# Performance work log

Measured on AMD Instinct MI355X. Metric: run time of the kernel, lower is better.

Reference implementation:

```python
import jax, jax.numpy as jnp
import numpy as np


def setup_inputs() -> dict:
    key = jax.random.key(0)
    k1, k2, k3, k4 = jax.random.split(key, 4)
    B, T, K = 256, 2048, 48
    logits = jax.random.normal(k1, (B, T, K), dtype=jnp.float32)
    transition_params = jax.random.normal(k2, (K, K), dtype=jnp.float32)
    targets = jax.random.randint(k3, (B, T), 0, K, dtype=jnp.int32)
    input_lengths = jax.random.randint(k4, (B,), 0, T, dtype=jnp.int32)
    return {"logits": logits, "transition_params": transition_params,
            "targets": targets, "input_lengths": input_lengths}


def _crf_log_likelihood(logits, transition_params, targets, input_lengths):
    B, T, K = logits.shape
    mask = (jnp.arange(T)[None, :] < input_lengths[:, None]).astype(logits.dtype)  # [B,T]

    # unary score: gather logits at target tags, masked sum over time
    unary = jnp.take_along_axis(logits, targets[..., None].astype(jnp.int32), axis=2)[..., 0]  # [B,T]
    unary_score = jnp.sum(unary * mask, axis=1)

    # binary score: transitions between consecutive tags, masked by mask[:,1:]
    binary = transition_params[targets[:, :-1], targets[:, 1:]]  # [B,T-1]
    binary_score = jnp.sum(binary * mask[:, 1:], axis=1)

    # log norm via forward algorithm (sequential logsumexp scan)
    alpha0 = logits[:, 0, :]  # [B,K]

    def step(alpha, logit_t):
        # alpha: [B,K] prev tag scores; logit_t: [B,K]
        scores = alpha[:, :, None] + transition_params[None, :, :]  # [B,K,K]
        new_alpha = logit_t + jax.nn.logsumexp(scores, axis=1)      # [B,K]
        return new_alpha, new_alpha

    _, alphas_rest = jax.lax.scan(step, alpha0, jnp.swapaxes(logits[:, 1:, :], 0, 1))
    all_alphas = jnp.concatenate([alpha0[None], alphas_rest], axis=0)  # [T,B,K]
    all_alphas = jnp.swapaxes(all_alphas, 0, 1)                        # [B,T,K]

    last_index = jnp.maximum(0, input_lengths - 1).astype(jnp.int32)   # [B]
    final_alpha = jnp.take_along_axis(all_alphas, last_index[:, None, None], axis=1)[:, 0, :]  # [B,K]
    log_norm = jax.nn.logsumexp(final_alpha, axis=1)
    log_norm = jnp.where(input_lengths <= 0, jnp.zeros_like(log_norm), log_norm)

    return unary_score + binary_score - log_norm  # [B]


def reference(logits, transition_params, targets, input_lengths):
    return _crf_log_likelihood(logits, transition_params, targets, input_lengths)
```

## Files before the change

kernel.cpp:

```cpp
#include <hip/hip_runtime.h>
#include <hip/hip_bf16.h>
#include <math.h>

#define TT   2048
#define KK   48
#define KP   68

typedef __attribute__((ext_vector_type(8))) short bf16x8;
typedef __attribute__((ext_vector_type(4))) float f32x4;
typedef __attribute__((ext_vector_type(2))) float f32x2;
typedef __attribute__((ext_vector_type(4))) unsigned int u32x4;
typedef unsigned short ushort_t;

union FragU { u32x4 u; bf16x8 h; };
union Q4   { f32x4 v; f32x2 h[2]; };

__device__ __forceinline__ float rlf(float x, int l) {
    return __uint_as_float((unsigned)__builtin_amdgcn_readlane((int)__float_as_uint(x), l));
}
__device__ __forceinline__ unsigned pk2(float a, float b) {
    __hip_bfloat162 h = __float22bfloat162_rn(make_float2(a, b));
    return *(unsigned*)&h;
}
__device__ __forceinline__ unsigned pk2a(float a, float b) {
    unsigned r;
    asm("v_cvt_pk_bf16_f32 %0, %1, %2" : "=v"(r) : "v"(a), "v"(b));
    return r;
}
__device__ __forceinline__ f32x2 pkmul(f32x2 a, f32x2 b) {
    f32x2 d;
    asm("v_pk_mul_f32 %0, %1, %2" : "=v"(d) : "v"(a), "v"(b));
    return d;
}

template <int SEGT, int NSEGT>
__global__ __launch_bounds__(64, 4) void crf_seg_kernel(
    const float* __restrict__ logits,
    const float* __restrict__ trans,
    const int*   __restrict__ lens,
    ushort_t*    __restrict__ Qout,
    float*       __restrict__ sigout)
{
    constexpr int NFULLT = NSEGT - 1;
    const int b    = blockIdx.x;
    const int seg  = blockIdx.y;
    const int job  = b * NSEGT + seg;
    const int lane = threadIdx.x;
    const int c = lane & 15, g = lane >> 4;

    int t0, t1;
    if (seg < NFULLT) { t0 = SEGT * seg + 1; t1 = SEGT * seg + SEGT; }
    else {
        int L  = lens[b];
        int nf = (L >= 2) ? (L - 1) / SEGT : 0;
        if (nf > NFULLT) nf = NFULLT;
        t0 = SEGT * nf + 1; t1 = L - 1;
    }

    __shared__ float    eLs[2][64];
    __shared__ ushort_t Qst[KK * KP];

    FragU A[3][2];
    #pragma unroll
    for (int mt = 0; mt < 3; ++mt) {
        const int r = 16 * mt + c;
        #pragma unroll
        for (int q = 0; q < 2; ++q) {
            #pragma unroll
            for (int ep = 0; ep < 4; ++ep) {
                float v0, v1;
                { int e = 2 * ep;     int kk = 32 * q + 16 * (e >> 2) + 4 * g + (e & 3);
                  v0 = (kk < KK) ? __expf(trans[kk * KK + r]) : 0.f; }
                { int e = 2 * ep + 1; int kk = 32 * q + 16 * (e >> 2) + 4 * g + (e & 3);
                  v1 = (kk < KK) ? __expf(trans[kk * KK + r]) : 0.f; }
                A[mt][q].u[ep] = pk2(v0, v1);
            }
        }
    }

    FragU Bf[3][2];
    #pragma unroll
    for (int nt = 0; nt < 3; ++nt) {
        const int n = 16 * nt + c;
        #pragma unroll
        for (int q = 0; q < 2; ++q) {
            #pragma unroll
            for (int ep = 0; ep < 4; ++ep) {
                int e0 = 2 * ep, e1 = 2 * ep + 1;
                int k0 = 32 * q + 16 * (e0 >> 2) + 4 * g + (e0 & 3);
                int k1 = 32 * q + 16 * (e1 >> 2) + 4 * g + (e1 & 3);
                unsigned lo = (k0 == n) ? 0x3F80u : 0u;
                unsigned hi = (k1 == n) ? 0x3F80u : 0u;
                Bf[nt][q].u[ep] = (hi << 16) | lo;
            }
        }
    }

    const float* lg_b = logits + (size_t)b * TT * KK;
    const int jj = (lane < KK) ? lane : 0;
    float sg = 0.f;
    const int nsteps = t1 - t0 + 1;

    f32x4 z4 = {0.f, 0.f, 0.f, 0.f};
    asm("" : "+v"(z4));

#define COLX(nt_, FIRST_)                                                     \
    {                                                                         \
        f32x4 y0 = __builtin_amdgcn_mfma_f32_16x16x32_bf16(                   \
                       A[0][0].h, Bf[nt_][0].h, z4, 0, 0, 0);                 \
        y0 = __builtin_amdgcn_mfma_f32_16x16x32_bf16(                         \
                       A[0][1].h, Bf[nt_][1].h, y0, 0, 0, 0);                 \
        f32x4 y1 = __builtin_amdgcn_mfma_f32_16x16x32_bf16(                   \
                       A[1][0].h, Bf[nt_][0].h, z4, 0, 0, 0);                 \
        y1 = __builtin_amdgcn_mfma_f32_16x16x32_bf16(                         \
                       A[1][1].h, Bf[nt_][1].h, y1, 0, 0, 0);                 \
        f32x4 y2 = __builtin_amdgcn_mfma_f32_16x16x32_bf16(                   \
                       A[2][0].h, Bf[nt_][0].h, z4, 0, 0, 0);                 \
        y2 = __builtin_amdgcn_mfma_f32_16x16x32_bf16(                         \
                       A[2][1].h, Bf[nt_][1].h, y2, 0, 0, 0);                 \
        if (FIRST_) {                                                         \
            float r = __uint_as_float((unsigned)                              \
                __builtin_amdgcn_readfirstlane((int)__float_as_uint(y0[0]))); \
            float rr = __builtin_amdgcn_rcpf(r);                              \
            sg += jk ? 0.f : __logf(r);                                       \
            rr2[0] = rr; rr2[1] = rr;                                         \
            { Q4 t_; t_.v = eL4[0]; es0.h[0] = pkmul(t_.h[0], rr2);           \
                                    es0.h[1] = pkmul(t_.h[1], rr2); }         \
            { Q4 t_; t_.v = eL4[1]; es1.h[0] = pkmul(t_.h[0], rr2);           \
                                    es1.h[1] = pkmul(t_.h[1], rr2); }         \
            { Q4 t_; t_.v = eL4[2]; es2.h[0] = pkmul(t_.h[0], rr2);           \
                                    es2.h[1] = pkmul(t_.h[1], rr2); }         \
        }                                                                     \
        Q4 q0_, q1_, q2_;                                                     \
        q0_.v = y0; q1_.v = y1; q2_.v = y2;                                   \
        f32x2 v00 = pkmul(q0_.h[0], es0.h[0]);                                \
        f32x2 v01 = pkmul(q0_.h[1], es0.h[1]);                                \
        f32x2 v10 = pkmul(q1_.h[0], es1.h[0]);                                \
        f32x2 v11 = pkmul(q1_.h[1], es1.h[1]);                                \
        f32x2 v20 = pkmul(q2_.h[0], es2.h[0]);                                \
        f32x2 v21 = pkmul(q2_.h[1], es2.h[1]);                                \
        unsigned w0 = pk2a(v00[0], v00[1]);                                   \
        unsigned w1 = pk2a(v01[0], v01[1]);                                   \
        unsigned w2 = pk2a(v10[0], v10[1]);                                   \
        unsigned w3 = pk2a(v11[0], v11[1]);                                   \
        unsigned w4 = pk2a(v20[0], v20[1]);                                   \
        unsigned w5 = pk2a(v21[0], v21[1]);                                   \
        if (G_) {                                                             \
            Bf[nt_][0].u[0] = jk ? Bf[nt_][0].u[0] : w0;                      \
            Bf[nt_][0].u[1] = jk ? Bf[nt_][0].u[1] : w1;                      \
            Bf[nt_][0].u[2] = jk ? Bf[nt_][0].u[2] : w2;                      \
            Bf[nt_][0].u[3] = jk ? Bf[nt_][0].u[3] : w3;                      \
            Bf[nt_][1].u[0] = jk ? Bf[nt_][1].u[0] : w4;                      \
            Bf[nt_][1].u[1] = jk ? Bf[nt_][1].u[1] : w5;                      \
        } else {                                                              \
            Bf[nt_][0].u[0] = w0; Bf[nt_][0].u[1] = w1;                       \
            Bf[nt_][0].u[2] = w2; Bf[nt_][0].u[3] = w3;                       \
            Bf[nt_][1].u[0] = w4; Bf[nt_][1].u[1] = w5;                       \
        }                                                                     \
        Bf[nt_][1].u[2] = 0u; Bf[nt_][1].u[3] = 0u;                           \
    }

#define STEP(u_, GG_)                                                         \
    {                                                                         \
        constexpr bool G_ = (GG_);                                            \
        const int i = 8 * cs + (u_);                                          \
        f32x4 eL4[3];                                                         \
        _Pragma("unroll")                                                     \
        for (int mt = 0; mt < 3; ++mt)                                        \
            eL4[mt] = *(const f32x4*)&eLs[par][16 * mt + 4 * g];              \
        float lgn = pf[((u_) + 1) & 7];                                       \
        int nr = t0 + i + 9; if (nr > TT - 1) nr = TT - 1;                    \
        pf[((u_) + 1) & 7] = lg_b[nr * KK + jj];                              \
        if (lane < KK) eLs[par ^ 1][lane] = __expf(lgn);                      \
        const bool jk = G_ ? (i >= nsteps) : false;                           \
        f32x2 rr2;                                                            \
        Q4 es0, es1, es2;                                                     \
        COLX(0, 1)                                                            \
        COLX(1, 0)                                                            \
        COLX(2, 0)                                                            \
        par ^= 1;                                                             \
    }

    int par = 0;
    if (nsteps > 0) {
        if (lane < KK) eLs[0][lane] = __expf(lg_b[t0 * KK + jj]);
        float pf[8];
        #pragma unroll
        for (int j = 1; j < 8; ++j) {
            int rj = t0 + j; if (rj > TT - 1) rj = TT - 1;
            pf[j] = lg_b[rj * KK + jj];
        }
        { int rj = t0 + 8; if (rj > TT - 1) rj = TT - 1; pf[0] = lg_b[rj * KK + jj]; }

        const int nchunks = (nsteps + 7) / 8;
        #pragma unroll 1
        for (int cs = 0; cs < nchunks - 1; ++cs) {
            STEP(0, false) STEP(1, false) STEP(2, false) STEP(3, false)
            STEP(4, false) STEP(5, false) STEP(6, false) STEP(7, false)
        }
        {
            const int cs = nchunks - 1;
            STEP(0, true) STEP(1, true) STEP(2, true) STEP(3, true)
            STEP(4, true) STEP(5, true) STEP(6, true) STEP(7, true)
        }
    }
#undef STEP
#undef COLX

    #pragma unroll
    for (int nt = 0; nt < 3; ++nt) {
        ushort_t* basep = &Qst[(16 * nt + c) * KP];
        *(unsigned*)&basep[4 * g]          = Bf[nt][0].u[0];
        *(unsigned*)&basep[4 * g + 2]      = Bf[nt][0].u[1];
        *(unsigned*)&basep[16 + 4 * g]     = Bf[nt][0].u[2];
        *(unsigned*)&basep[16 + 4 * g + 2] = Bf[nt][0].u[3];
        *(unsigned*)&basep[32 + 4 * g]     = Bf[nt][1].u[0];
        *(unsigned*)&basep[32 + 4 * g + 2] = Bf[nt][1].u[1];
    }
    __syncthreads();

    if (lane < KK) {
        const int m = lane;
        unsigned w[24];
        #pragma unroll
        for (int np = 0; np < 24; ++np) {
            unsigned lo = Qst[(2 * np)     * KP + m];
            unsigned hi = Qst[(2 * np + 1) * KP + m];
            w[np] = (hi << 16) | lo;
        }
        ushort_t* dst = Qout + (size_t)job * (KK * KK) + m * KK;
        #pragma unroll
        for (int i4 = 0; i4 < 6; ++i4) {
            uint4 o; o.x = w[4*i4]; o.y = w[4*i4+1]; o.z = w[4*i4+2]; o.w = w[4*i4+3];
            *(uint4*)&dst[8 * i4] = o;
        }
    }
    if (lane == 0) sigout[job] = sg;
}

template <int SEGT, int NSEGT>
__global__ __launch_bounds__(64) void crf_comb_kernel(
    const float* __restrict__ logits, const float* __restrict__ trans,
    const int* __restrict__ targets, const int* __restrict__ lens,
    const ushort_t* __restrict__ Qall, const float* __restrict__ sig,
    float* __restrict__ out)
{
    constexpr int NFULLT = NSEGT - 1;
    const int b = blockIdx.x, lane = threadIdx.x;
    const int jj = (lane < KK) ? lane : 0;
    const int L = lens[b];

    __shared__ float s_trans[KK * KK];
    for (int k = lane; k < KK * KK; k += 64) s_trans[k] = trans[k];
    __syncthreads();

    const float* lg_b = logits  + (size_t)b * TT * KK;
    const int*   tg_b = targets + (size_t)b * TT;

    float ub = 0.f;
    #pragma unroll 4
    for (int t = lane; t < TT; t += 64) {
        if (t < L) {
            int tg = tg_b[t];
            ub += lg_b[t * KK + tg];
            if (t >= 1) { int tp = tg_b[t - 1]; ub += s_trans[tp * KK + tg]; }
        }
    }
    #pragma unroll
    for (int d = 32; d >= 1; d >>= 1) ub += __shfl_xor(ub, d, 64);

    float log_norm = 0.f;
    if (L > 0) {
        float a0 = lg_b[jj];
        float M  = rlf(a0, 0);
        float s  = (lane < KK) ? __expf(a0 - M) : 0.f;
        int nf = (L >= 2) ? (L - 1) / SEGT : 0;
        if (nf > NFULLT) nf = NFULLT;

        for (int ci = 0; ci <= nf; ++ci) {
            const int job = b * NSEGT + ((ci < nf) ? ci : NFULLT);
            const ushort_t* Qr = Qall + (size_t)job * (KK * KK) + jj * KK;
            unsigned rw[24];
            #pragma unroll
            for (int i4 = 0; i4 < 6; ++i4) {
                uint4 v = *(const uint4*)&Qr[8 * i4];
                rw[4*i4] = v.x; rw[4*i4+1] = v.y; rw[4*i4+2] = v.z; rw[4*i4+3] = v.w;
            }
            float acc = 0.f;
            #pragma unroll
            for (int ip = 0; ip < 24; ++ip) {
                unsigned u = rw[ip];
                float q0 = __uint_as_float(u << 16);
                float q1 = __uint_as_float(u & 0xFFFF0000u);
                acc = fmaf(rlf(s, 2 * ip),     q0, acc);
                acc = fmaf(rlf(s, 2 * ip + 1), q1, acc);
            }
            float r  = rlf(acc, 0);
            float rr = __builtin_amdgcn_rcpf(r);
            s = (lane < KK) ? acc * rr : 0.f;
            M += __logf(r) + sig[job];
        }

        float ssum = (lane < KK) ? s : 0.f;
        #pragma unroll
        for (int d = 32; d >= 1; d >>= 1) ssum += __shfl_xor(ssum, d, 64);
        log_norm = M + __logf(ssum);
    }

    if (lane == 0) out[b] = (L <= 0) ? 0.f : (ub - log_norm);
}

__global__ __launch_bounds__(64) void crf_fwd_fallback(
    const float* __restrict__ logits, const float* __restrict__ trans,
    const int* __restrict__ targets, const int* __restrict__ lens,
    float* __restrict__ out)
{
    const int b = blockIdx.x, lane = threadIdx.x;
    const int jj = (lane < KK) ? lane : 0;
    const int L = lens[b];
    __shared__ float s_trans[KK * KK];
    for (int k = lane; k < KK * KK; k += 64) s_trans[k] = trans[k];
    float et[KK];
    #pragma unroll
    for (int i = 0; i < KK; ++i) et[i] = __expf(trans[i * KK + jj]);
    __syncthreads();
    const float* lg_b = logits + (size_t)b * TT * KK;
    const int* tg_b = targets + (size_t)b * TT;
    float ub = 0.f;
    for (int t = lane; t < TT; t += 64) {
        if (t < L) {
            int tg = tg_b[t];
            ub += lg_b[t * KK + tg];
            if (t >= 1) { int tp = tg_b[t - 1]; ub += s_trans[tp * KK + tg]; }
        }
    }
    #pragma unroll
    for (int d = 32; d >= 1; d >>= 1) ub += __shfl_xor(ub, d, 64);
    float a0 = lg_b[jj];
    float M = rlf(a0, 0);
    float s = (lane < KK) ? __expf(a0 - M) : 0.f;
    float sC = s, MC = M;
    const int Lm1 = L - 1;
    float pf[8];
    #pragma unroll
    for (int u = 0; u < 8; ++u) pf[u] = lg_b[(1 + u) * KK + jj];
    #pragma unroll 1
    for (int cc = 0; cc < 256; ++cc) {
        #pragma unroll
        for (int u = 0; u < 8; ++u) {
            const int t = 1 + cc * 8 + u;
            float lg = pf[u];
            int nrow = t + 8; if (nrow > TT - 1) nrow = TT - 1;
            pf[u] = lg_b[nrow * KK + jj];
            float eL = __expf(lg);
            float ac0 = 0.f, ac1 = 0.f, ac2 = 0.f, ac3 = 0.f;
            #pragma unroll
            for (int i = 0; i < KK; i += 4) {
                float s0 = rlf(s, i), s1 = rlf(s, i+1), s2 = rlf(s, i+2), s3 = rlf(s, i+3);
                ac0 = fmaf(s0, et[i], ac0);   ac1 = fmaf(s1, et[i+1], ac1);
                ac2 = fmaf(s2, et[i+2], ac2); ac3 = fmaf(s3, et[i+3], ac3);
            }
            float e = ((ac0 + ac1) + (ac2 + ac3)) * eL;
            bool cap = (t == Lm1);
            sC = cap ? e : sC;  MC = cap ? M : MC;
            float r = rlf(e, 0);
            s = e * __builtin_amdgcn_rcpf(r);
            M += __logf(r);
        }
    }
    float ssum = (lane < KK) ? sC : 0.f;
    #pragma unroll
    for (int d = 32; d >= 1; d >>= 1) ssum += __shfl_xor(ssum, d, 64);
    float log_norm = MC + __logf(ssum);
    if (lane == 0) out[b] = (L <= 0) ? 0.f : (ub - log_norm);
}

extern "C" void kernel_launch(void* const* d_in, const int* in_sizes, int n_in,
                              void* d_out, int out_size, void* d_ws, size_t ws_size,
                              hipStream_t stream) {
    const float* logits  = (const float*)d_in[0];
    const float* trans   = (const float*)d_in[1];
    const int*   targets = (const int*)  d_in[2];
    const int*   lens    = (const int*)  d_in[3];
    float*       out     = (float*)d_out;
    const int B = in_sizes[3];

    const size_t q64  = (size_t)B * 32 * KK * KK * sizeof(ushort_t);
    const size_t n64  = q64 + (size_t)B * 32 * sizeof(float);
    const size_t q128 = (size_t)B * 16 * KK * KK * sizeof(ushort_t);
    const size_t n128 = q128 + (size_t)B * 16 * sizeof(float);

    if (ws_size >= n64) {
        ushort_t* Qout = (ushort_t*)d_ws;
        float*    sig  = (float*)((char*)d_ws + q64);
        crf_seg_kernel<64, 32><<<dim3(B, 32), 64, 0, stream>>>(logits, trans, lens, Qout, sig);
        crf_comb_kernel<64, 32><<<B, 64, 0, stream>>>(logits, trans, targets, lens, Qout, sig, out);
    } else if (ws_size >= n128) {
        ushort_t* Qout = (ushort_t*)d_ws;
        float*    sig  = (float*)((char*)d_ws + q128);
        crf_seg_kernel<128, 16><<<dim3(B, 16), 64, 0, stream>>>(logits, trans, lens, Qout, sig);
        crf_comb_kernel<128, 16><<<B, 64, 0, stream>>>(logits, trans, targets, lens, Qout, sig, out);
    } else {
        crf_fwd_fallback<<<B, 64, 0, stream>>>(logits, trans, targets, lens, out);
    }
}
```

Before: 187.9 us.

## Split segment transfer-matrix columns across three blocks for more parallelism

Each segment block previously propagated all 48 columns of the segment transfer matrix. Now a third grid dimension splits them into three 16-column slices, each in its own wavefront with its own per-column scale. The combine kernel folds the per-slice log scales back in by rescaling each row with exp(sg_w - sg_0). This triples the block count and cuts the serial MFMA chain per step, aiming to shorten the critical path and raise occupancy. The cost is that logits loads and exponentials are repeated three times, and there is some numerical risk from the per-slice scale differences.

```diff
diff --git a/kernel.cpp b/kernel.cpp
--- a/kernel.cpp
+++ b/kernel.cpp
@@ -4,7 +4,7 @@
 
 #define TT   2048
 #define KK   48
-#define KP   68
+#define KP2  52
 
 typedef __attribute__((ext_vector_type(8))) short bf16x8;
 typedef __attribute__((ext_vector_type(4))) float f32x4;
@@ -44,6 +44,7 @@
     constexpr int NFULLT = NSEGT - 1;
     const int b    = blockIdx.x;
     const int seg  = blockIdx.y;
+    const int wst  = blockIdx.z;
     const int job  = b * NSEGT + seg;
     const int lane = threadIdx.x;
     const int c = lane & 15, g = lane >> 4;
@@ -58,7 +59,7 @@
     }
 
     __shared__ float    eLs[2][64];
-    __shared__ ushort_t Qst[KK * KP];
+    __shared__ ushort_t Qst[16 * KP2];
 
     FragU A[3][2];
     #pragma unroll
@@ -78,10 +79,9 @@
         }
     }
 
-    FragU Bf[3][2];
-    #pragma unroll
-    for (int nt = 0; nt < 3; ++nt) {
-        const int n = 16 * nt + c;
+    FragU Bf[2];
+    {
+        const int n = 16 * wst + c;
         #pragma unroll
         for (int q = 0; q < 2; ++q) {
             #pragma unroll
@@ -91,7 +91,7 @@
                 int k1 = 32 * q + 16 * (e1 >> 2) + 4 * g + (e1 & 3);
                 unsigned lo = (k0 == n) ? 0x3F80u : 0u;
                 unsigned hi = (k1 == n) ? 0x3F80u : 0u;
-                Bf[nt][q].u[ep] = (hi << 16) | lo;
+                Bf[q].u[ep] = (hi << 16) | lo;
             }
         }
     }
@@ -104,80 +104,63 @@
     f32x4 z4 = {0.f, 0.f, 0.f, 0.f};
     asm("" : "+v"(z4));
 
-#define COLX(nt_, FIRST_)                                                     \
-    {                                                                         \
-        f32x4 y0 = __builtin_amdgcn_mfma_f32_16x16x32_bf16(                   \
-                       A[0][0].h, Bf[nt_][0].h, z4, 0, 0, 0);                 \
-        y0 = __builtin_amdgcn_mfma_f32_16x16x32_bf16(                         \
-                       A[0][1].h, Bf[nt_][1].h, y0, 0, 0, 0);                 \
-        f32x4 y1 = __builtin_amdgcn_mfma_f32_16x16x32_bf16(                   \
-                       A[1][0].h, Bf[nt_][0].h, z4, 0, 0, 0);                 \
-        y1 = __builtin_amdgcn_mfma_f32_16x16x32_bf16(                         \
-                       A[1][1].h, Bf[nt_][1].h, y1, 0, 0, 0);                 \
-        f32x4 y2 = __builtin_amdgcn_mfma_f32_16x16x32_bf16(                   \
-                       A[2][0].h, Bf[nt_][0].h, z4, 0, 0, 0);                 \
-        y2 = __builtin_amdgcn_mfma_f32_16x16x32_bf16(                         \
-                       A[2][1].h, Bf[nt_][1].h, y2, 0, 0, 0);                 \
-        if (FIRST_) {                                                         \
-            float r = __uint_as_float((unsigned)                              \
-                __builtin_amdgcn_readfirstlane((int)__float_as_uint(y0[0]))); \
-            float rr = __builtin_amdgcn_rcpf(r);                              \
-            sg += jk ? 0.f : __logf(r);                                       \
-            rr2[0] = rr; rr2[1] = rr;                                         \
-            { Q4 t_; t_.v = eL4[0]; es0.h[0] = pkmul(t_.h[0], rr2);           \
-                                    es0.h[1] = pkmul(t_.h[1], rr2); }         \
-            { Q4 t_; t_.v = eL4[1]; es1.h[0] = pkmul(t_.h[0], rr2);           \
-                                    es1.h[1] = pkmul(t_.h[1], rr2); }         \
-            { Q4 t_; t_.v = eL4[2]; es2.h[0] = pkmul(t_.h[0], rr2);           \
-                                    es2.h[1] = pkmul(t_.h[1], rr2); }         \
-        }                                                                     \
-        Q4 q0_, q1_, q2_;                                                     \
-        q0_.v = y0; q1_.v = y1; q2_.v = y2;                                   \
-        f32x2 v00 = pkmul(q0_.h[0], es0.h[0]);                                \
-        f32x2 v01 = pkmul(q0_.h[1], es0.h[1]);                                \
-        f32x2 v10 = pkmul(q1_.h[0], es1.h[0]);                                \
-        f32x2 v11 = pkmul(q1_.h[1], es1.h[1]);                                \
-        f32x2 v20 = pkmul(q2_.h[0], es2.h[0]);                                \
-        f32x2 v21 = pkmul(q2_.h[1], es2.h[1]);                                \
-        unsigned w0 = pk2a(v00[0], v00[1]);                                   \
-        unsigned w1 = pk2a(v01[0], v01[1]);                                   \
-        unsigned w2 = pk2a(v10[0], v10[1]);                                   \
-        unsigned w3 = pk2a(v11[0], v11[1]);                                   \
-        unsigned w4 = pk2a(v20[0], v20[1]);                                   \
-        unsigned w5 = pk2a(v21[0], v21[1]);                                   \
-        if (G_) {                                                             \
-            Bf[nt_][0].u[0] = jk ? Bf[nt_][0].u[0] : w0;                      \
-            Bf[nt_][0].u[1] = jk ? Bf[nt_][0].u[1] : w1;                      \
-            Bf[nt_][0].u[2] = jk ? Bf[nt_][0].u[2] : w2;                      \
-            Bf[nt_][0].u[3] = jk ? Bf[nt_][0].u[3] : w3;                      \
-            Bf[nt_][1].u[0] = jk ? Bf[nt_][1].u[0] : w4;                      \
-            Bf[nt_][1].u[1] = jk ? Bf[nt_][1].u[1] : w5;                      \
-        } else {                                                              \
-            Bf[nt_][0].u[0] = w0; Bf[nt_][0].u[1] = w1;                       \
-            Bf[nt_][0].u[2] = w2; Bf[nt_][0].u[3] = w3;                       \
-            Bf[nt_][1].u[0] = w4; Bf[nt_][1].u[1] = w5;                       \
-        }                                                                     \
-        Bf[nt_][1].u[2] = 0u; Bf[nt_][1].u[3] = 0u;                           \
-    }
-
 #define STEP(u_, GG_)                                                         \
     {                                                                         \
         constexpr bool G_ = (GG_);                                            \
         const int i = 8 * cs + (u_);                                          \
-        f32x4 eL4[3];                                                         \
-        _Pragma("unroll")                                                     \
-        for (int mt = 0; mt < 3; ++mt)                                        \
-            eL4[mt] = *(const f32x4*)&eLs[par][16 * mt + 4 * g];              \
+        f32x4 eL4_0 = *(const f32x4*)&eLs[par][4 * g];                        \
+        f32x4 eL4_1 = *(const f32x4*)&eLs[par][16 + 4 * g];                   \
+        f32x4 eL4_2 = *(const f32x4*)&eLs[par][32 + 4 * g];                   \
         float lgn = pf[((u_) + 1) & 7];                                       \
         int nr = t0 + i + 9; if (nr > TT - 1) nr = TT - 1;                    \
         pf[((u_) + 1) & 7] = lg_b[nr * KK + jj];                              \
         if (lane < KK) eLs[par ^ 1][lane] = __expf(lgn);                      \
         const bool jk = G_ ? (i >= nsteps) : false;                           \
-        f32x2 rr2;                                                            \
-        Q4 es0, es1, es2;                                                     \
-        COLX(0, 1)                                                            \
-        COLX(1, 0)                                                            \
-        COLX(2, 0)                                                            \
+        f32x4 y0 = __builtin_amdgcn_mfma_f32_16x16x32_bf16(                   \
+                       A[0][0].h, Bf[0].h, z4, 0, 0, 0);                      \
+        y0 = __builtin_amdgcn_mfma_f32_16x16x32_bf16(                         \
+                       A[0][1].h, Bf[1].h, y0, 0, 0, 0);                      \
+        f32x4 y1 = __builtin_amdgcn_mfma_f32_16x16x32_bf16(                   \
+                       A[1][0].h, Bf[0].h, z4, 0, 0, 0);                      \
+        y1 = __builtin_amdgcn_mfma_f32_16x16x32_bf16(                         \
+                       A[1][1].h, Bf[1].h, y1, 0, 0, 0);                      \
+        f32x4 y2 = __builtin_amdgcn_mfma_f32_16x16x32_bf16(                   \
+                       A[2][0].h, Bf[0].h, z4, 0, 0, 0);                      \
+        y2 = __builtin_amdgcn_mfma_f32_16x16x32_bf16(                         \
+                       A[2][1].h, Bf[1].h, y2, 0, 0, 0);                      \
+        float r = __uint_as_float((unsigned)__builtin_amdgcn_readfirstlane(   \
+                      (int)__float_as_uint(y0[0])));                          \
+        float rr = __builtin_amdgcn_rcpf(r);                                  \
+        sg += jk ? 0.f : __logf(r);                                           \
+        f32x2 rr2; rr2[0] = rr; rr2[1] = rr;                                  \
+        Q4 q0_, q1_, q2_, e0_, e1_, e2_;                                      \
+        e0_.v = eL4_0; e1_.v = eL4_1; e2_.v = eL4_2;                          \
+        q0_.v = y0; q1_.v = y1; q2_.v = y2;                                   \
+        f32x2 es00 = pkmul(e0_.h[0], rr2), es01 = pkmul(e0_.h[1], rr2);       \
+        f32x2 es10 = pkmul(e1_.h[0], rr2), es11 = pkmul(e1_.h[1], rr2);       \
+        f32x2 es20 = pkmul(e2_.h[0], rr2), es21 = pkmul(e2_.h[1], rr2);       \
+        f32x2 v00 = pkmul(q0_.h[0], es00), v01 = pkmul(q0_.h[1], es01);       \
+        f32x2 v10 = pkmul(q1_.h[0], es10), v11 = pkmul(q1_.h[1], es11);       \
+        f32x2 v20 = pkmul(q2_.h[0], es20), v21 = pkmul(q2_.h[1], es21);       \
+        unsigned nw0 = pk2a(v00[0], v00[1]);                                  \
+        unsigned nw1 = pk2a(v01[0], v01[1]);                                  \
+        unsigned nw2 = pk2a(v10[0], v10[1]);                                  \
+        unsigned nw3 = pk2a(v11[0], v11[1]);                                  \
+        unsigned nw4 = pk2a(v20[0], v20[1]);                                  \
+        unsigned nw5 = pk2a(v21[0], v21[1]);                                  \
+        if (G_) {                                                             \
+            Bf[0].u[0] = jk ? Bf[0].u[0] : nw0;                               \
+            Bf[0].u[1] = jk ? Bf[0].u[1] : nw1;                               \
+            Bf[0].u[2] = jk ? Bf[0].u[2] : nw2;                               \
+            Bf[0].u[3] = jk ? Bf[0].u[3] : nw3;                               \
+            Bf[1].u[0] = jk ? Bf[1].u[0] : nw4;                               \
+            Bf[1].u[1] = jk ? Bf[1].u[1] : nw5;                               \
+        } else {                                                              \
+            Bf[0].u[0] = nw0; Bf[0].u[1] = nw1;                               \
+            Bf[0].u[2] = nw2; Bf[0].u[3] = nw3;                               \
+            Bf[1].u[0] = nw4; Bf[1].u[1] = nw5;                               \
+        }                                                                     \
+        Bf[1].u[2] = 0u; Bf[1].u[3] = 0u;                                     \
         par ^= 1;                                                             \
     }
 
@@ -205,37 +188,34 @@
         }
     }
 #undef STEP
-#undef COLX
-
-    #pragma unroll
-    for (int nt = 0; nt < 3; ++nt) {
-        ushort_t* basep = &Qst[(16 * nt + c) * KP];
-        *(unsigned*)&basep[4 * g]          = Bf[nt][0].u[0];
-        *(unsigned*)&basep[4 * g + 2]      = Bf[nt][0].u[1];
-        *(unsigned*)&basep[16 + 4 * g]     = Bf[nt][0].u[2];
-        *(unsigned*)&basep[16 + 4 * g + 2] = Bf[nt][0].u[3];
-        *(unsigned*)&basep[32 + 4 * g]     = Bf[nt][1].u[0];
-        *(unsigned*)&basep[32 + 4 * g + 2] = Bf[nt][1].u[1];
+
+    {
+        ushort_t* basep = &Qst[c * KP2];
+        *(unsigned*)&basep[4 * g]          = Bf[0].u[0];
+        *(unsigned*)&basep[4 * g + 2]      = Bf[0].u[1];
+        *(unsigned*)&basep[16 + 4 * g]     = Bf[0].u[2];
+        *(unsigned*)&basep[16 + 4 * g + 2] = Bf[0].u[3];
+        *(unsigned*)&basep[32 + 4 * g]     = Bf[1].u[0];
+        *(unsigned*)&basep[32 + 4 * g + 2] = Bf[1].u[1];
     }
     __syncthreads();
 
     if (lane < KK) {
         const int m = lane;
-        unsigned w[24];
-        #pragma unroll
-        for (int np = 0; np < 24; ++np) {
-            unsigned lo = Qst[(2 * np)     * KP + m];
-            unsigned hi = Qst[(2 * np + 1) * KP + m];
-            w[np] = (hi << 16) | lo;
-        }
-        ushort_t* dst = Qout + (size_t)job * (KK * KK) + m * KK;
-        #pragma unroll
-        for (int i4 = 0; i4 < 6; ++i4) {
-            uint4 o; o.x = w[4*i4]; o.y = w[4*i4+1]; o.z = w[4*i4+2]; o.w = w[4*i4+3];
-            *(uint4*)&dst[8 * i4] = o;
-        }
-    }
-    if (lane == 0) sigout[job] = sg;
+        unsigned wv[8];
+        #pragma unroll
+        for (int np = 0; np < 8; ++np) {
+            unsigned lo = Qst[(2 * np)     * KP2 + m];
+            unsigned hi = Qst[(2 * np + 1) * KP2 + m];
+            wv[np] = (hi << 16) | lo;
+        }
+        ushort_t* dst = Qout + (size_t)job * (KK * KK) + m * KK + 16 * wst;
+        uint4 o0; o0.x = wv[0]; o0.y = wv[1]; o0.z = wv[2]; o0.w = wv[3];
+        uint4 o1; o1.x = wv[4]; o1.y = wv[5]; o1.z = wv[6]; o1.w = wv[7];
+        *(uint4*)&dst[0] = o0;
+        *(uint4*)&dst[8] = o1;
+    }
+    if (lane == 0) sigout[job * 3 + wst] = sg;
 }
 
 template <int SEGT, int NSEGT>
@@ -295,10 +275,12 @@
                 acc = fmaf(rlf(s, 2 * ip),     q0, acc);
                 acc = fmaf(rlf(s, 2 * ip + 1), q1, acc);
             }
+            float sgw = sig[job * 3 + (jj >> 4)];
+            float sg0 = rlf(sgw, 0);
             float r  = rlf(acc, 0);
             float rr = __builtin_amdgcn_rcpf(r);
-            s = (lane < KK) ? acc * rr : 0.f;
-            M += __logf(r) + sig[job];
+            s = (lane < KK) ? acc * __expf(sgw - sg0) * rr : 0.f;
+            M += __logf(r) + sg0;
         }
 
         float ssum = (lane < KK) ? s : 0.f;
@@ -386,19 +368,19 @@
     const int B = in_sizes[3];
 
     const size_t q64  = (size_t)B * 32 * KK * KK * sizeof(ushort_t);
-    const size_t n64  = q64 + (size_t)B * 32 * sizeof(float);
+    const size_t n64  = q64 + (size_t)B * 32 * 3 * sizeof(float);
     const size_t q128 = (size_t)B * 16 * KK * KK * sizeof(ushort_t);
-    const size_t n128 = q128 + (size_t)B * 16 * sizeof(float);
+    const size_t n128 = q128 + (size_t)B * 16 * 3 * sizeof(float);
 
     if (ws_size >= n64) {
         ushort_t* Qout = (ushort_t*)d_ws;
         float*    sig  = (float*)((char*)d_ws + q64);
-        crf_seg_kernel<64, 32><<<dim3(B, 32), 64, 0, stream>>>(logits, trans, lens, Qout, sig);
+        crf_seg_kernel<64, 32><<<dim3(B, 32, 3), 64, 0, stream>>>(logits, trans, lens, Qout, sig);
         crf_comb_kernel<64, 32><<<B, 64, 0, stream>>>(logits, trans, targets, lens, Qout, sig, out);
     } else if (ws_size >= n128) {
         ushort_t* Qout = (ushort_t*)d_ws;
         float*    sig  = (float*)((char*)d_ws + q128);
-        crf_seg_kernel<128, 16><<<dim3(B, 16), 64, 0, stream>>>(logits, trans, lens, Qout, sig);
+        crf_seg_kernel<128, 16><<<dim3(B, 16, 3), 64, 0, stream>>>(logits, trans, lens, Qout, sig);
         crf_comb_kernel<128, 16><<<B, 64, 0, stream>>>(logits, trans, targets, lens, Qout, sig, out);
     } else {
         crf_fwd_fallback<<<B, 64, 0, stream>>>(logits, trans, targets, lens, out);
```

Measured after the change: 234.1 us. +24.5%, slower.
